# Kernel tuning notes

Hardware: AMD Instinct MI355X
Metric: run time of the kernel (lower is better)

## Reference

```python
import jax, jax.numpy as jnp
import numpy as np
from jax.scipy.special import erf

NPT = 65536          # number of depos
P = 14               # static patch extent per axis: floor(2*nsigma*sigma_max/h)+2 with sigma_max=1.0, h=0.5
NSIGMA = 3.0
SPACING = np.array([0.5, 0.5, 0.5], dtype=np.float32)  # grid spacing per axis [mm]


def setup_inputs() -> dict:
    key = jax.random.key(0)
    k1, k2, k3, k4 = jax.random.split(key, 4)
    sigma = 0.2 + 0.8 * jax.random.uniform(k1, (NPT, 3), dtype=jnp.float32)   # diffusion widths in [0.2,1.0] mm
    time = 10.0 * jax.random.uniform(k2, (NPT,), dtype=jnp.float32)           # drift-time coordinate (grid units of distance after transform)
    charge = 1000.0 * jax.random.uniform(k3, (NPT,), dtype=jnp.float32)       # ionization charge per depo
    tail = 10.0 * jax.random.normal(k4, (NPT, 3), dtype=jnp.float32)          # depo points (npt, 3)
    return {"sigma": sigma, "time": time, "charge": charge, "tail": tail}


def _raster_depos(spacing, centers, sigma, charge):
    """Integrated-Gaussian rasterization of depos onto per-depo grid patches.

    spacing: (3,)   centers/sigma: (npt,3)   charge: (npt,)
    Returns rasters (npt, P, P, P) and integer grid offsets (npt, 3).
    """
    sqrt2 = jnp.sqrt(jnp.float32(2.0))
    # lowest grid cell touched by the +-nsigma extent, per depo, per axis
    imin = jnp.floor((centers - NSIGMA * sigma) / spacing)            # (npt, 3)
    k = jnp.arange(P + 1, dtype=jnp.float32)                          # cell edge indices
    edges = (imin[:, :, None] + k) * spacing[None, :, None]           # (npt, 3, P+1)
    z = (edges - centers[:, :, None]) / (sqrt2 * sigma[:, :, None])
    cdf = 0.5 * erf(z)                                                # gaussian CDF (up to constant)
    q = cdf[..., 1:] - cdf[..., :-1]                                  # per-cell 1D integrated fraction (npt, 3, P)
    # separable 3D splat: outer product of the three 1D profiles, scaled by charge
    rasters = jnp.einsum('n,ni,nj,nk->nijk', charge, q[:, 0], q[:, 1], q[:, 2])
    return rasters, imin.astype(jnp.int32)


def reference(sigma, time, charge, tail):
    spacing = jnp.asarray(SPACING)
    # Raster._transform with pdims=(1,2), tdim=-1: axes=[1,2]; axes.insert(-1,0) -> [1,0,2];
    # then the tdim(=-1) column is overwritten with `time`.
    centers = jnp.stack([tail[:, 1], tail[:, 0], time], axis=-1)      # (npt, 3)
    rasters, offsets = _raster_depos(spacing, centers, sigma, charge)
    return rasters, offsets
```

## Files before the change

kernel.cpp:

```cpp
#include <hip/hip_runtime.h>
#include <hip/hip_bf16.h>

#define NPT 65536
#define PATCH 14
#define CELLS (PATCH * PATCH * PATCH)
#define VEC4S (CELLS / 4)
#define NSIGMA 3.0f
#define INV_SPACING 2.0f
#define SPACING_F 0.5f
#define SQRT2 1.41421356237309504880f

__global__ __launch_bounds__(256) void raster_kernel(
    const float* __restrict__ sigma,
    const float* __restrict__ time,
    const float* __restrict__ charge,
    const float* __restrict__ tail,
    float* __restrict__ out_rast,
    float* __restrict__ out_off)
{
    const int n = blockIdx.x;
    const int t = threadIdx.x;

    __shared__ float cdf[3][16];
    __shared__ float q[3][16];

    if (t < 45) {
        const int a = t / 15;
        const int e = t - a * 15;
        const float sig = sigma[n * 3 + a];
        float c;
        if (a == 0)      c = tail[n * 3 + 1];
        else if (a == 1) c = tail[n * 3 + 0];
        else             c = time[n];
        const float im = floorf((c - NSIGMA * sig) * INV_SPACING);
        const float edge = (im + (float)e) * SPACING_F;
        const float z = (edge - c) / (SQRT2 * sig);
        cdf[a][e] = 0.5f * erff(z);
        if (e == 0) {
            out_off[n * 3 + a] = im;
        }
    }
    __syncthreads();

    if (t < 42) {
        const int a = t / 14;
        const int c = t - a * 14;
        float qq = cdf[a][c + 1] - cdf[a][c];
        if (a == 0) qq *= charge[n];
        q[a][c] = qq;
    }
    __syncthreads();

    float4* __restrict__ out4 = (float4*)(out_rast + (size_t)n * CELLS);
    for (int c4 = t; c4 < VEC4S; c4 += 256) {
        const int base = c4 * 4;
        float4 v;
        float* vp = &v.x;
#pragma unroll
        for (int u = 0; u < 4; ++u) {
            const int cell = base + u;
            const int i = cell / (PATCH * PATCH);
            const int r = cell - i * (PATCH * PATCH);
            const int j = r / PATCH;
            const int k = r - j * PATCH;
            vp[u] = q[0][i] * q[1][j] * q[2][k];
        }
        out4[c4] = v;
    }
}

extern "C" void kernel_launch(void* const* d_in, const int* in_sizes, int n_in,
                              void* d_out, int out_size, void* d_ws, size_t ws_size,
                              hipStream_t stream) {
    const float* sigma  = (const float*)d_in[0];
    const float* time_  = (const float*)d_in[1];
    const float* charge = (const float*)d_in[2];
    const float* tail   = (const float*)d_in[3];

    float* out_rast = (float*)d_out;
    float* out_off  = (float*)d_out + (size_t)NPT * CELLS;

    raster_kernel<<<NPT, 256, 0, stream>>>(sigma, time_, charge, tail, out_rast, out_off);
}
```

Baseline: 738.3 us.

## Assign one depo per wavefront, shuffle CDF differences, use nontemporal stores

Each 256-thread block now handles four depos, one per 64-lane wavefront, instead of one depo per block. That cuts the grid to a quarter of its size and gives each wave its own shared q profile. The CDF difference is computed with a lane shuffle rather than a second shared-memory pass, which removes one barrier. Raster output is written with nontemporal vector stores to avoid cache pollution on this write-bound kernel.

```diff
diff --git a/kernel.cpp b/kernel.cpp
--- a/kernel.cpp
+++ b/kernel.cpp
@@ -5,57 +5,52 @@
 #define PATCH 14
 #define CELLS (PATCH * PATCH * PATCH)
 #define VEC4S (CELLS / 4)
-#define NSIGMA 3.0f
-#define INV_SPACING 2.0f
-#define SPACING_F 0.5f
-#define SQRT2 1.41421356237309504880f
+
+typedef float f4 __attribute__((ext_vector_type(4)));
 
 __global__ __launch_bounds__(256) void raster_kernel(
     const float* __restrict__ sigma,
-    const float* __restrict__ time,
+    const float* __restrict__ time_,
     const float* __restrict__ charge,
     const float* __restrict__ tail,
     float* __restrict__ out_rast,
     float* __restrict__ out_off)
 {
-    const int n = blockIdx.x;
-    const int t = threadIdx.x;
+    const int lane = threadIdx.x & 63;
+    const int wv   = threadIdx.x >> 6;
+    const int n    = (blockIdx.x << 2) | wv;
 
-    __shared__ float cdf[3][16];
-    __shared__ float q[3][16];
+    __shared__ float q_s[4][3][16];
 
-    if (t < 45) {
-        const int a = t / 15;
-        const int e = t - a * 15;
-        const float sig = sigma[n * 3 + a];
-        float c;
-        if (a == 0)      c = tail[n * 3 + 1];
-        else if (a == 1) c = tail[n * 3 + 0];
-        else             c = time[n];
-        const float im = floorf((c - NSIGMA * sig) * INV_SPACING);
-        const float edge = (im + (float)e) * SPACING_F;
-        const float z = (edge - c) / (SQRT2 * sig);
-        cdf[a][e] = 0.5f * erff(z);
-        if (e == 0) {
-            out_off[n * 3 + a] = im;
+    {
+        int a = lane / 15;
+        int e = lane - a * 15;
+        int ac = (a < 3) ? a : 2;
+        float sig = sigma[n * 3 + ac];
+        float c = (ac == 0) ? tail[n * 3 + 1]
+                : (ac == 1) ? tail[n * 3 + 0]
+                            : time_[n];
+        float im   = floorf((c - 3.0f * sig) * 2.0f);
+        float edge = (im + (float)e) * 0.5f;
+        float z    = (edge - c) / (1.41421356237f * sig);
+        float cdf  = 0.5f * erff(z);
+        float cdfn = __shfl_down(cdf, 1);
+        if (a < 3) {
+            if (e == 0) out_off[n * 3 + a] = im;
+            if (e < 14) {
+                float qq = cdfn - cdf;
+                if (a == 0) qq *= charge[n];
+                q_s[wv][a][e] = qq;
+            }
         }
     }
     __syncthreads();
 
-    if (t < 42) {
-        const int a = t / 14;
-        const int c = t - a * 14;
-        float qq = cdf[a][c + 1] - cdf[a][c];
-        if (a == 0) qq *= charge[n];
-        q[a][c] = qq;
-    }
-    __syncthreads();
-
-    float4* __restrict__ out4 = (float4*)(out_rast + (size_t)n * CELLS);
-    for (int c4 = t; c4 < VEC4S; c4 += 256) {
+    const float* qw = &q_s[wv][0][0];
+    f4* __restrict__ out4 = (f4*)(out_rast + (size_t)n * CELLS);
+    for (int c4 = lane; c4 < VEC4S; c4 += 64) {
         const int base = c4 * 4;
-        float4 v;
-        float* vp = &v.x;
+        f4 v;
 #pragma unroll
         for (int u = 0; u < 4; ++u) {
             const int cell = base + u;
@@ -63,9 +58,9 @@
             const int r = cell - i * (PATCH * PATCH);
             const int j = r / PATCH;
             const int k = r - j * PATCH;
-            vp[u] = q[0][i] * q[1][j] * q[2][k];
+            v[u] = qw[i] * qw[16 + j] * qw[32 + k];
         }
-        out4[c4] = v;
+        __builtin_nontemporal_store(v, &out4[c4]);
     }
 }
 
@@ -80,5 +75,5 @@
     float* out_rast = (float*)d_out;
     float* out_off  = (float*)d_out + (size_t)NPT * CELLS;
 
-    raster_kernel<<<NPT, 256, 0, stream>>>(sigma, time_, charge, tail, out_rast, out_off);
+    raster_kernel<<<NPT / 4, 256, 0, stream>>>(sigma, time_, charge, tail, out_rast, out_off);
 }
```

After: 730.8 us. Within noise of the previous version (-1.0%).
